# Kernel tuning notes

Measured on AMD Instinct MI355X. Metric: run time of the kernel, lower is better.

The kernel has to match this reference:

```python
import jax, jax.numpy as jnp
import numpy as np

B, I, R, L, U = 256, 512, 1024, 2, 11  # batch, input_size, rnn_size, num_layers, num_unroll


def setup_inputs() -> dict:
    key = jax.random.key(0)
    ks = jax.random.split(key, 10)
    s = 0.02
    return {
        "x": jax.random.normal(ks[0], (B, I), jnp.float32),
        "init_states_input": jax.random.normal(ks[1], (B, 2 * L * R), jnp.float32),
        # per-unroll (NOT shared) weights, stacked along unroll dim U
        "Wi0": jax.random.normal(ks[2], (U, 4 * R, I), jnp.float32) * s,
        "bi0": jax.random.normal(ks[3], (U, 4 * R), jnp.float32) * s,
        "Wh0": jax.random.normal(ks[4], (U, 4 * R, R), jnp.float32) * s,
        "bh0": jax.random.normal(ks[5], (U, 4 * R), jnp.float32) * s,
        "Wi1": jax.random.normal(ks[6], (U, 4 * R, R), jnp.float32) * s,
        "bi1": jax.random.normal(ks[7], (U, 4 * R), jnp.float32) * s,
        "Wh1": jax.random.normal(ks[8], (U, 4 * R, R), jnp.float32) * s,
        "bh1": jax.random.normal(ks[9], (U, 4 * R), jnp.float32) * s,
    }


def _cell(pre, c_prev):
    # torch chunk(4, dim=1) order: in_gate, forget_gate, out_gate, in_transform
    i, f, o, g = jnp.split(pre, 4, axis=1)
    c = jax.nn.sigmoid(f) * c_prev + jax.nn.sigmoid(i) * jnp.tanh(g)
    h = jax.nn.sigmoid(o) * jnp.tanh(c)
    return h, c


def reference(x, init_states_input, Wi0, bi0, Wh0, bh0, Wi1, bi1, Wh1, bh1):
    st = init_states_input.reshape(B, 2 * L, R)
    # chunk order: [h0, c0, h1, c1]
    h0, c0, h1, c1 = st[:, 0], st[:, 1], st[:, 2], st[:, 3]

    def step(carry, p):
        h0, c0, h1, c1 = carry
        wi0, vbi0, wh0, vbh0, wi1, vbi1, wh1, vbh1 = p
        out_prev = h1  # original appends now_hs[i][-1]: top-layer h BEFORE this step
        pre0 = x @ wi0.T + vbi0 + h0 @ wh0.T + vbh0  # [B, 4R]
        h0n, c0n = _cell(pre0, c0)
        pre1 = h0n @ wi1.T + vbi1 + h1 @ wh1.T + vbh1
        h1n, c1n = _cell(pre1, c1)
        return (h0n, c0n, h1n, c1n), out_prev

    _, ys = jax.lax.scan(step, (h0, c0, h1, c1),
                         (Wi0, bi0, Wh0, bh0, Wi1, bi1, Wh1, bh1))
    # ys: [U, B, R]; torch.cat along dim 1 in unroll order -> [B, U*R]
    return jnp.transpose(ys, (1, 0, 2)).reshape(B, U * R)
```

## Files before the change

kernel.cpp:

```cpp
#include <hip/hip_runtime.h>
#include <hip/hip_bf16.h>

#define B_N 256
#define R_N 1024
#define U_N 11
#define BK 32
#define SP 40

typedef __attribute__((ext_vector_type(8))) short bf16x8;
typedef __attribute__((ext_vector_type(4))) float f32x4;

__device__ __forceinline__ float sigmoid_f(float x) {
    return 1.0f / (1.0f + __expf(-x));
}

__device__ __forceinline__ float tanh_f(float x) {
    x = fminf(15.0f, fmaxf(-15.0f, x));
    const float e = __expf(2.0f * x);
    return (e - 1.0f) / (e + 1.0f);
}

__device__ __forceinline__ short bf16_of(float x) {
    union { __hip_bfloat16 h; short s; } u;
    u.h = __float2bfloat16(x);
    return u.s;
}

__device__ __forceinline__ short4 pack4(float4 v) {
    short4 r;
    r.x = bf16_of(v.x); r.y = bf16_of(v.y);
    r.z = bf16_of(v.z); r.w = bf16_of(v.w);
    return r;
}

__global__ __launch_bounds__(512, 4) void lstm_layer(
    const float* __restrict__ A1, int lda1, int K1, const float* __restrict__ W1,
    const float* __restrict__ A2, int lda2, int K2, const float* __restrict__ W2,
    const float* __restrict__ bi, const float* __restrict__ bh,
    float* __restrict__ c_state,
    float* __restrict__ h_out, int ldh)
{
    __shared__ __align__(16) char smem_raw[30720];

    const int tid  = threadIdx.x;
    const int lane = tid & 63;
    const int wave = tid >> 6;
    const int group = wave >> 2;
    const int gate  = wave & 3;
    const int ln   = lane & 15;
    const int quad = lane >> 4;
    const int lk   = quad * 8;
    const int tg   = tid & 255;

    const int m_base = blockIdx.y * 32;
    const int rb     = blockIdx.x * 16;

    const int Ktot  = K1 + K2;
    const int Khalf = Ktot >> 1;
    const int NC    = Khalf / BK;

    const int arow = tg >> 3;
    const int acol = (tg & 7) * 4;

    const float* baseA1 = A1 + (size_t)(m_base + arow) * lda1 + acol;
    const float* baseA2 = A2 + (size_t)(m_base + arow) * lda2 + acol;
    const float* baseW1[2];
    const float* baseW2[2];
#pragma unroll
    for (int l = 0; l < 2; ++l) {
        const int wrow = l * 32 + (tg >> 3);
        const int g = wrow >> 4, rr = wrow & 15;
        baseW1[l] = W1 + (size_t)(g * R_N + rb + rr) * K1 + acol;
        baseW2[l] = W2 + (size_t)(g * R_N + rb + rr) * K2 + acol;
    }

    f32x4 acc[2];
#pragma unroll
    for (int mf = 0; mf < 2; ++mf) {
        f32x4 z = {0.0f, 0.0f, 0.0f, 0.0f};
        acc[mf] = z;
    }

    float4 pA;
    float4 pW[2];
    auto load_chunk = [&](int c) {
        const int kv = group * Khalf + c * BK;
        if (kv < K1) {
            pA = *reinterpret_cast<const float4*>(baseA1 + kv);
#pragma unroll
            for (int l = 0; l < 2; ++l)
                pW[l] = *reinterpret_cast<const float4*>(baseW1[l] + kv);
        } else {
            const int kc = kv - K1;
            pA = *reinterpret_cast<const float4*>(baseA2 + kc);
#pragma unroll
            for (int l = 0; l < 2; ++l)
                pW[l] = *reinterpret_cast<const float4*>(baseW2[l] + kc);
        }
    };

    auto body = [&](int c, int buf) {
        short* sAb = reinterpret_cast<short*>(&smem_raw[(size_t)(buf * 2 + group) * 2560]);
        short* sWb = reinterpret_cast<short*>(&smem_raw[10240 + (size_t)(buf * 2 + group) * 5120]);

        *reinterpret_cast<short4*>(&sAb[arow * SP + acol]) = pack4(pA);
#pragma unroll
        for (int l = 0; l < 2; ++l) {
            const int wrow = l * 32 + (tg >> 3);
            *reinterpret_cast<short4*>(&sWb[wrow * SP + acol]) = pack4(pW[l]);
        }

        __syncthreads();

        if (c + 1 < NC) load_chunk(c + 1);

        bf16x8 af[2], wf;
#pragma unroll
        for (int mf = 0; mf < 2; ++mf)
            af[mf] = *reinterpret_cast<const bf16x8*>(&sAb[(mf * 16 + ln) * SP + lk]);
        wf = *reinterpret_cast<const bf16x8*>(&sWb[(gate * 16 + ln) * SP + lk]);

        acc[0] = __builtin_amdgcn_mfma_f32_16x16x32_bf16(af[0], wf, acc[0], 0, 0, 0);
        acc[1] = __builtin_amdgcn_mfma_f32_16x16x32_bf16(af[1], wf, acc[1], 0, 0, 0);
    };

    load_chunk(0);
#pragma unroll 1
    for (int c = 0; c < NC; c += 2) {
        body(c, 0);
        body(c + 1, 1);
    }

    __syncthreads();
    float* sPre = reinterpret_cast<float*>(smem_raw);

#pragma unroll
    for (int mf = 0; mf < 2; ++mf)
#pragma unroll
        for (int t = 0; t < 4; ++t) {
            const int m = mf * 16 + quad * 4 + t;
            sPre[group * 2048 + (gate * 32 + m) * 16 + ln] = acc[mf][t];
        }
    __syncthreads();

    {
        const int m = tid >> 4;
        const int r = tid & 15;
        const int gm = m_base + m;
        const int gr = rb + r;
        const float pI = sPre[(0 * 32 + m) * 16 + r] + sPre[2048 + (0 * 32 + m) * 16 + r]
                       + bi[0 * R_N + gr] + bh[0 * R_N + gr];
        const float pF = sPre[(1 * 32 + m) * 16 + r] + sPre[2048 + (1 * 32 + m) * 16 + r]
                       + bi[1 * R_N + gr] + bh[1 * R_N + gr];
        const float pO = sPre[(2 * 32 + m) * 16 + r] + sPre[2048 + (2 * 32 + m) * 16 + r]
                       + bi[2 * R_N + gr] + bh[2 * R_N + gr];
        const float pG = sPre[(3 * 32 + m) * 16 + r] + sPre[2048 + (3 * 32 + m) * 16 + r]
                       + bi[3 * R_N + gr] + bh[3 * R_N + gr];
        const size_t cidx = (size_t)gm * R_N + gr;
        const float cv = sigmoid_f(pF) * c_state[cidx] + sigmoid_f(pI) * tanh_f(pG);
        c_state[cidx] = cv;
        h_out[(size_t)gm * ldh + gr] = sigmoid_f(pO) * tanh_f(cv);
    }
}

__global__ __launch_bounds__(256) void init_states(
    const float* __restrict__ st, float* __restrict__ h0,
    float* __restrict__ c0, float* __restrict__ c1, float* __restrict__ out)
{
    const int idx = blockIdx.x * 256 + threadIdx.x;
    const int b = idx >> 10;
    const int r = idx & 1023;
    const float* s = st + (size_t)b * 4096;
    h0[idx] = s[r];
    c0[idx] = s[1024 + r];
    out[(size_t)b * (U_N * R_N) + r] = s[2048 + r];
    c1[idx] = s[3072 + r];
}

extern "C" void kernel_launch(void* const* d_in, const int* in_sizes, int n_in,
                              void* d_out, int out_size, void* d_ws, size_t ws_size,
                              hipStream_t stream)
{
    const float* x   = (const float*)d_in[0];
    const float* st  = (const float*)d_in[1];
    const float* Wi0 = (const float*)d_in[2];
    const float* bi0 = (const float*)d_in[3];
    const float* Wh0 = (const float*)d_in[4];
    const float* bh0 = (const float*)d_in[5];
    const float* Wi1 = (const float*)d_in[6];
    const float* bi1 = (const float*)d_in[7];
    const float* Wh1 = (const float*)d_in[8];
    const float* bh1 = (const float*)d_in[9];
    float* out = (float*)d_out;

    float* h0a = (float*)d_ws;
    float* h0b = h0a + B_N * R_N;
    float* c0  = h0b + B_N * R_N;
    float* c1  = c0 + B_N * R_N;

    init_states<<<dim3((B_N * R_N) / 256), 256, 0, stream>>>(st, h0a, c0, c1, out);

    const dim3 grid(R_N / 16, B_N / 32);
    for (int u = 0; u < 10; ++u) {
        const float* h0_in = (u & 1) ? h0b : h0a;
        float* h0_out      = (u & 1) ? h0a : h0b;
        lstm_layer<<<grid, 512, 0, stream>>>(
            x, 512, 512, Wi0 + (size_t)u * 4096 * 512,
            h0_in, R_N, R_N, Wh0 + (size_t)u * 4096 * 1024,
            bi0 + (size_t)u * 4096, bh0 + (size_t)u * 4096,
            c0, h0_out, R_N);
        lstm_layer<<<grid, 512, 0, stream>>>(
            h0_out, R_N, R_N, Wi1 + (size_t)u * 4096 * 1024,
            out + (size_t)u * R_N, U_N * R_N, R_N, Wh1 + (size_t)u * 4096 * 1024,
            bi1 + (size_t)u * 4096, bh1 + (size_t)u * 4096,
            c1, out + (size_t)(u + 1) * R_N, U_N * R_N);
    }
}
```

Before: 1.450 ms.

## Retile LSTM GEMM to 128 batch rows by 8 units, dropping split-K

Each block now computes all four gates for 8 hidden units across 128 batch rows, with every wave covering the full K range instead of splitting K between two groups. This cuts how many blocks re-read the same fp32 weight rows, lowering global weight traffic, which likely dominates. In exchange each block runs a K loop twice as long with no split-K parallelism, reads activations more redundantly, and drops the occupancy hint from launch bounds.

```diff
diff --git a/kernel.cpp b/kernel.cpp
--- a/kernel.cpp
+++ b/kernel.cpp
@@ -6,6 +6,7 @@
 #define U_N 11
 #define BK 32
 #define SP 40
+#define SPP 33
 
 typedef __attribute__((ext_vector_type(8))) short bf16x8;
 typedef __attribute__((ext_vector_type(4))) float f32x4;
@@ -33,95 +34,85 @@
     return r;
 }
 
-__global__ __launch_bounds__(512, 4) void lstm_layer(
+__global__ __launch_bounds__(512) void lstm_layer(
     const float* __restrict__ A1, int lda1, int K1, const float* __restrict__ W1,
     const float* __restrict__ A2, int lda2, int K2, const float* __restrict__ W2,
     const float* __restrict__ bi, const float* __restrict__ bh,
     float* __restrict__ c_state,
     float* __restrict__ h_out, int ldh)
 {
-    __shared__ __align__(16) char smem_raw[30720];
+    __shared__ __align__(16) char smem_raw[25600];
 
     const int tid  = threadIdx.x;
     const int lane = tid & 63;
     const int wave = tid >> 6;
-    const int group = wave >> 2;
-    const int gate  = wave & 3;
     const int ln   = lane & 15;
     const int quad = lane >> 4;
     const int lk   = quad * 8;
-    const int tg   = tid & 255;
-
-    const int m_base = blockIdx.y * 32;
-    const int rb     = blockIdx.x * 16;
-
-    const int Ktot  = K1 + K2;
-    const int Khalf = Ktot >> 1;
-    const int NC    = Khalf / BK;
-
-    const int arow = tg >> 3;
-    const int acol = (tg & 7) * 4;
-
-    const float* baseA1 = A1 + (size_t)(m_base + arow) * lda1 + acol;
-    const float* baseA2 = A2 + (size_t)(m_base + arow) * lda2 + acol;
-    const float* baseW1[2];
-    const float* baseW2[2];
-#pragma unroll
-    for (int l = 0; l < 2; ++l) {
-        const int wrow = l * 32 + (tg >> 3);
-        const int g = wrow >> 4, rr = wrow & 15;
-        baseW1[l] = W1 + (size_t)(g * R_N + rb + rr) * K1 + acol;
-        baseW2[l] = W2 + (size_t)(g * R_N + rb + rr) * K2 + acol;
-    }
+
+    const int m_base = blockIdx.y * 128;
+    const int rb8    = blockIdx.x * 8;
+
+    const int Ktot = K1 + K2;
+    const int NC   = Ktot / BK;
+
+    const int arow = tid >> 3;
+    const int acol = (tid & 7) * 4;
+    const int wrow = tid >> 3;
+    const int wcol = (tid & 7) * 4;
+    const int wgate = wrow >> 3;
+    const int wcig  = wrow & 7;
+
+    const float* baseA1r0 = A1 + (size_t)(m_base + arow) * lda1 + acol;
+    const float* baseA1r1 = A1 + (size_t)(m_base + arow + 64) * lda1 + acol;
+    const float* baseA2r0 = A2 + (size_t)(m_base + arow) * lda2 + acol;
+    const float* baseA2r1 = A2 + (size_t)(m_base + arow + 64) * lda2 + acol;
+    const float* baseW1 = W1 + (size_t)(wgate * R_N + rb8 + wcig) * K1 + wcol;
+    const float* baseW2 = W2 + (size_t)(wgate * R_N + rb8 + wcig) * K2 + wcol;
 
     f32x4 acc[2];
 #pragma unroll
-    for (int mf = 0; mf < 2; ++mf) {
+    for (int rf = 0; rf < 2; ++rf) {
         f32x4 z = {0.0f, 0.0f, 0.0f, 0.0f};
-        acc[mf] = z;
-    }
-
-    float4 pA;
-    float4 pW[2];
+        acc[rf] = z;
+    }
+
+    float4 pA0, pA1, pW;
+
     auto load_chunk = [&](int c) {
-        const int kv = group * Khalf + c * BK;
+        const int kv = c * BK;
         if (kv < K1) {
-            pA = *reinterpret_cast<const float4*>(baseA1 + kv);
-#pragma unroll
-            for (int l = 0; l < 2; ++l)
-                pW[l] = *reinterpret_cast<const float4*>(baseW1[l] + kv);
+            pA0 = *reinterpret_cast<const float4*>(baseA1r0 + kv);
+            pA1 = *reinterpret_cast<const float4*>(baseA1r1 + kv);
+            if (tid < 256) pW = *reinterpret_cast<const float4*>(baseW1 + kv);
         } else {
             const int kc = kv - K1;
-            pA = *reinterpret_cast<const float4*>(baseA2 + kc);
-#pragma unroll
-            for (int l = 0; l < 2; ++l)
-                pW[l] = *reinterpret_cast<const float4*>(baseW2[l] + kc);
+            pA0 = *reinterpret_cast<const float4*>(baseA2r0 + kc);
+            pA1 = *reinterpret_cast<const float4*>(baseA2r1 + kc);
+            if (tid < 256) pW = *reinterpret_cast<const float4*>(baseW2 + kc);
         }
     };
 
     auto body = [&](int c, int buf) {
-        short* sAb = reinterpret_cast<short*>(&smem_raw[(size_t)(buf * 2 + group) * 2560]);
-        short* sWb = reinterpret_cast<short*>(&smem_raw[10240 + (size_t)(buf * 2 + group) * 5120]);
-
-        *reinterpret_cast<short4*>(&sAb[arow * SP + acol]) = pack4(pA);
-#pragma unroll
-        for (int l = 0; l < 2; ++l) {
-            const int wrow = l * 32 + (tg >> 3);
-            *reinterpret_cast<short4*>(&sWb[wrow * SP + acol]) = pack4(pW[l]);
-        }
+        short* sAb = reinterpret_cast<short*>(&smem_raw[(size_t)buf * 10240]);
+        short* sWb = reinterpret_cast<short*>(&smem_raw[20480 + (size_t)buf * 2560]);
+
+        *reinterpret_cast<short4*>(&sAb[arow * SP + acol]) = pack4(pA0);
+        *reinterpret_cast<short4*>(&sAb[(arow + 64) * SP + acol]) = pack4(pA1);
+        if (tid < 256)
+            *reinterpret_cast<short4*>(&sWb[wrow * SP + wcol]) = pack4(pW);
 
         __syncthreads();
 
         if (c + 1 < NC) load_chunk(c + 1);
 
-        bf16x8 af[2], wf;
-#pragma unroll
-        for (int mf = 0; mf < 2; ++mf)
-            af[mf] = *reinterpret_cast<const bf16x8*>(&sAb[(mf * 16 + ln) * SP + lk]);
-        wf = *reinterpret_cast<const bf16x8*>(&sWb[(gate * 16 + ln) * SP + lk]);
-
-        acc[0] = __builtin_amdgcn_mfma_f32_16x16x32_bf16(af[0], wf, acc[0], 0, 0, 0);
-        acc[1] = __builtin_amdgcn_mfma_f32_16x16x32_bf16(af[1], wf, acc[1], 0, 0, 0);
+        bf16x8 af, wf0, wf1;
+        af  = *reinterpret_cast<const bf16x8*>(&sAb[(wave * 16 + ln) * SP + lk]);
+        wf0 = *reinterpret_cast<const bf16x8*>(&sWb[ln * SP + lk]);
+        wf1 = *reinterpret_cast<const bf16x8*>(&sWb[(16 + ln) * SP + lk]);
+
+        acc[0] = __builtin_amdgcn_mfma_f32_16x16x32_bf16(af, wf0, acc[0], 0, 0, 0);
+        acc[1] = __builtin_amdgcn_mfma_f32_16x16x32_bf16(af, wf1, acc[1], 0, 0, 0);
     };
 
     load_chunk(0);
@@ -135,27 +126,23 @@
     float* sPre = reinterpret_cast<float*>(smem_raw);
 
 #pragma unroll
-    for (int mf = 0; mf < 2; ++mf)
-#pragma unroll
-        for (int t = 0; t < 4; ++t) {
-            const int m = mf * 16 + quad * 4 + t;
-            sPre[group * 2048 + (gate * 32 + m) * 16 + ln] = acc[mf][t];
-        }
+    for (int rf = 0; rf < 2; ++rf)
+#pragma unroll
+        for (int t = 0; t < 4; ++t)
+            sPre[(wave * 16 + quad * 4 + t) * SPP + rf * 16 + ln] = acc[rf][t];
     __syncthreads();
 
-    {
-        const int m = tid >> 4;
-        const int r = tid & 15;
+#pragma unroll
+    for (int i = 0; i < 2; ++i) {
+        const int ci = tid + i * 512;
+        const int m = ci >> 3;
+        const int j = ci & 7;
         const int gm = m_base + m;
-        const int gr = rb + r;
-        const float pI = sPre[(0 * 32 + m) * 16 + r] + sPre[2048 + (0 * 32 + m) * 16 + r]
-                       + bi[0 * R_N + gr] + bh[0 * R_N + gr];
-        const float pF = sPre[(1 * 32 + m) * 16 + r] + sPre[2048 + (1 * 32 + m) * 16 + r]
-                       + bi[1 * R_N + gr] + bh[1 * R_N + gr];
-        const float pO = sPre[(2 * 32 + m) * 16 + r] + sPre[2048 + (2 * 32 + m) * 16 + r]
-                       + bi[2 * R_N + gr] + bh[2 * R_N + gr];
-        const float pG = sPre[(3 * 32 + m) * 16 + r] + sPre[2048 + (3 * 32 + m) * 16 + r]
-                       + bi[3 * R_N + gr] + bh[3 * R_N + gr];
+        const int gr = rb8 + j;
+        const float pI = sPre[m * SPP + 0 * 8 + j] + bi[0 * R_N + gr] + bh[0 * R_N + gr];
+        const float pF = sPre[m * SPP + 1 * 8 + j] + bi[1 * R_N + gr] + bh[1 * R_N + gr];
+        const float pO = sPre[m * SPP + 2 * 8 + j] + bi[2 * R_N + gr] + bh[2 * R_N + gr];
+        const float pG = sPre[m * SPP + 3 * 8 + j] + bi[3 * R_N + gr] + bh[3 * R_N + gr];
         const size_t cidx = (size_t)gm * R_N + gr;
         const float cv = sigmoid_f(pF) * c_state[cidx] + sigmoid_f(pI) * tanh_f(pG);
         c_state[cidx] = cv;
@@ -200,7 +187,7 @@
 
     init_states<<<dim3((B_N * R_N) / 256), 256, 0, stream>>>(st, h0a, c0, c1, out);
 
-    const dim3 grid(R_N / 16, B_N / 32);
+    const dim3 grid(R_N / 8, B_N / 128);
     for (int u = 0; u < 10; ++u) {
         const float* h0_in = (u & 1) ? h0b : h0a;
         float* h0_out      = (u & 1) ? h0a : h0b;
```

New measurement: 1.336 ms. 7.9% less time.
